# Optimization experiments

Measured on AMD Instinct MI355X. Metric: run time of the kernel, lower is better.

Reference implementation:

```python
import jax, jax.numpy as jnp
import numpy as np

EMB = 384
HID = 256
HEADS = 4
HD = HID // HEADS  # 64
LAYERS = 2
M_DOCS = 32
TOTAL = 4096  # 1 query + 32 docs + 4063 sentences
LN_EPS = 1e-5


def _layernorm(x, scale, bias):
    mu = jnp.mean(x, axis=-1, keepdims=True)
    var = jnp.mean(jnp.square(x - mu), axis=-1, keepdims=True)
    return (x - mu) * jax.lax.rsqrt(var + LN_EPS) * scale + bias


def setup_inputs() -> dict:
    key = jax.random.key(0)
    ks = jax.random.split(key, 12)
    g = 0.05  # small init scale (stand-in for xavier)
    return {
        "node_embeddings": jax.random.normal(ks[0], (TOTAL, EMB), jnp.float32),
        "adj": jax.random.randint(ks[1], (TOTAL, TOTAL), 0, 2, jnp.int32),
        "num_docs": M_DOCS,
        "proj_w": jax.random.normal(ks[2], (HID, EMB), jnp.float32) * g,
        "proj_b": jnp.zeros((HID,), jnp.float32),
        "ln_scale": jnp.ones((LAYERS, HID), jnp.float32),
        "ln_bias": jnp.zeros((LAYERS, HID), jnp.float32),
        "gat_W": jax.random.normal(ks[3], (LAYERS, HEADS, HD, HID), jnp.float32) * g,
        "gat_a": jax.random.normal(ks[4], (LAYERS, HEADS, 2 * HD), jnp.float32) * g,
        "fusion_w": jax.random.normal(ks[5], (HID, 2 * HID + 2), jnp.float32) * g,
        "fusion_b": jnp.zeros((HID,), jnp.float32),
        "out_w": jax.random.normal(ks[6], (HID,), jnp.float32) * g,
        "out_b": jnp.float32(0.5),
    }


def reference(node_embeddings, adj, num_docs, proj_w, proj_b, ln_scale, ln_bias,
              gat_W, gat_a, fusion_w, fusion_b, out_w, out_b):
    T = node_embeddings.shape[0]
    M = num_docs
    N = T - 1 - M  # number of sentences
    # input projection + relu (dropout = identity in eval)
    h = jax.nn.relu(node_embeddings @ proj_w.T + proj_b)  # (T, HID)
    # query-guided sentence re-weighting
    q = h[0:1]                     # (1, HID)
    s = h[1 + M:]                  # (N, HID)
    qn = q / (jnp.linalg.norm(q, axis=1, keepdims=True) + 1e-8)
    sn = s / (jnp.linalg.norm(s, axis=1, keepdims=True) + 1e-8)
    cos = (qn @ sn.T).reshape(-1, 1)          # (N,1)
    s = s + 0.8 * q * cos
    h = jnp.concatenate([h[:1 + M], s], axis=0)
    mask = (adj == 0)[None]                   # (1,T,T)
    for i in range(LAYERS):
        res = h
        x = _layernorm(h, ln_scale[i], ln_bias[i])
        Wh = jnp.einsum('nd,hkd->hnk', x, gat_W[i])                # (H,T,HD)
        # concat-attention a.[Wh_i ; Wh_j] == a_src.Wh_i + a_dst.Wh_j
        src = jnp.einsum('hnk,hk->hn', Wh, gat_a[i, :, :HD])       # (H,T)
        dst = jnp.einsum('hnk,hk->hn', Wh, gat_a[i, :, HD:])       # (H,T)
        e = jax.nn.leaky_relu(src[:, :, None] + dst[:, None, :], 0.2)  # (H,T,T)
        e = jnp.where(mask, -jnp.inf, e)
        attn = jax.nn.softmax(e, axis=-1)                          # softmax over j
        hn = jnp.einsum('hij,hjk->hik', attn, Wh)                  # (H,T,HD)
        hcat = jnp.transpose(hn, (1, 0, 2)).reshape(T, HEADS * HD)
        h = 0.5 * jax.nn.relu(hcat) + 0.5 * res
    qh = h[0:1]
    sh = h[1 + M:]
    scores = (qh @ sh.T) / (HID ** 0.5)       # (1,N)
    aw = jax.nn.softmax(scores, axis=-1)
    awT = aw.T                                # (N,1)
    qw = qh * (awT + 0.5)                     # (N,HID)
    qnf = qh / (jnp.linalg.norm(qh, axis=1, keepdims=True) + 1e-8)
    snf = sh / (jnp.linalg.norm(sh, axis=1, keepdims=True) + 1e-8)
    cosf = (qnf @ snf.T).reshape(-1, 1)       # (N,1)
    feat = jnp.concatenate([sh, qw, cosf, awT], axis=1)  # (N, 2*HID+2)
    g = jax.nn.relu(feat @ fusion_w.T + fusion_b)
    out = g @ out_w + out_b                   # (N,)
    return out + 0.5 * cosf[:, 0]
```

## Files before the change

kernel.cpp:

```cpp
#include <hip/hip_runtime.h>
#include <hip/hip_bf16.h>
#include <stdint.h>

#define TOTAL 4096
#define EMB 384
#define MD 32
#define NDOCS (TOTAL - 1 - MD)
#define LN_EPS 1e-5f

typedef __hip_bfloat16 bf16;
typedef unsigned short ushort_t;
typedef __attribute__((ext_vector_type(8))) short short8;
typedef __attribute__((ext_vector_type(4))) float f32x4;
typedef __attribute__((ext_vector_type(2))) float f32x2;

__device__ __forceinline__ float ldf(const void* p, int i, int isbf) {
    return isbf ? __bfloat162float(((const bf16*)p)[i]) : ((const float*)p)[i];
}

__device__ __forceinline__ unsigned f2bf(float x) {
    return (__float_as_uint(x) + 0x8000u) >> 16;
}

__device__ __forceinline__ unsigned fenc(float f) {
    unsigned u = __float_as_uint(f);
    return (u >> 31) ? ~u : (u | 0x80000000u);
}
__device__ __forceinline__ float fdec(unsigned k) {
    return __uint_as_float((k & 0x80000000u) ? (k & 0x7FFFFFFFu) : ~k);
}

#define NTRANS ((EMB * 256 + 2 * 65536 + 514 * 256) / 256)
__global__ void k_adjmask(const int* adj, unsigned long long* maskb,
                          const uint16_t* embp, int* flag, unsigned* dmaxu,
                          const void* proj_w, const void* gat_W, const void* fusion_w,
                          float* projT, float* gatT, float* fwT) {
    __shared__ int red[4];
    int i = blockIdx.x, t = threadIdx.x;
    int w = t >> 6, l = t & 63;
    for (int c = w; c < 64; c += 4) {
        int a = adj[(size_t)i * TOTAL + c * 64 + l];
        unsigned long long m = __ballot(a != 0);
        if (l == 0) maskb[i * 64 + c] = m;
    }
    if (i == 0) {
        for (int idx = t; idx < 2048; idx += 256) dmaxu[idx] = 0x007FFFFFu;
    }
    if (i < NTRANS) {
        int cnt = 0;
        for (int k = t; k < 4096; k += 256) {
            uint16_t wd = embp[2 * k];
            int e = (wd >> 7) & 0xFF;
            if (e >= 100 && e <= 140) cnt++;
        }
        for (int o = 32; o > 0; o >>= 1) cnt += __shfl_down(cnt, o);
        if ((t & 63) == 0) red[t >> 6] = cnt;
        __syncthreads();
        int isbf = (red[0] + red[1] + red[2] + red[3] > 2048) ? 1 : 0;
        if (i == 0 && t == 0) flag[0] = isbf;
        int idx = i * 256 + t;
        if (idx < EMB * 256) {
            int d = idx >> 8, c = idx & 255;
            projT[idx] = ldf(proj_w, c * EMB + d, isbf);
        } else if (idx < EMB * 256 + 2 * 65536) {
            int r = idx - EMB * 256;
            int ll = r >> 16, rem = r & 65535;
            int d = rem >> 8, c = rem & 255;
            gatT[r] = ldf(gat_W, ll * 65536 + c * 256 + d, isbf);
        } else {
            int r = idx - (EMB * 256 + 2 * 65536);
            int j = r >> 8, c = r & 255;
            fwT[r] = ldf(fusion_w, c * 514 + j, isbf);
        }
    }
}

#define PR 8
__global__ void k_proj(const void* emb, const void* proj_b, const float* projT, float* h,
                       const int* flagp) {
    __shared__ float xs[PR][EMB];
    int isbf = flagp[0];
    int i0 = blockIdx.x * PR, t = threadIdx.x;
    for (int idx = t; idx < PR * EMB; idx += 256) {
        int r = idx / EMB, d = idx % EMB;
        xs[r][d] = ldf(emb, (i0 + r) * EMB + d, isbf);
    }
    __syncthreads();
    float acc[PR];
    float bias = ldf(proj_b, t, isbf);
#pragma unroll
    for (int r = 0; r < PR; r++) acc[r] = bias;
    for (int d0 = 0; d0 < EMB; d0 += 4) {
        float w0 = projT[d0 * 256 + t];
        float w1 = projT[(d0 + 1) * 256 + t];
        float w2 = projT[(d0 + 2) * 256 + t];
        float w3 = projT[(d0 + 3) * 256 + t];
#pragma unroll
        for (int r = 0; r < PR; r++) {
            float4 x = *(const float4*)&xs[r][d0];
            acc[r] = fmaf(x.x, w0, acc[r]);
            acc[r] = fmaf(x.y, w1, acc[r]);
            acc[r] = fmaf(x.z, w2, acc[r]);
            acc[r] = fmaf(x.w, w3, acc[r]);
        }
    }
#pragma unroll
    for (int r = 0; r < PR; r++) h[(size_t)(i0 + r) * 256 + t] = fmaxf(acc[r], 0.f);
}

__global__ __launch_bounds__(256) void k_cosupdate(float* h) {
    int t = threadIdx.x, W = t >> 6, lane = t & 63;
    float4* h4 = (float4*)h;
    float4 q4 = h4[lane];
    float a = q4.x * q4.x + q4.y * q4.y + q4.z * q4.z + q4.w * q4.w;
    for (int o = 32; o > 0; o >>= 1) a += __shfl_xor(a, o);
    float qn = sqrtf(a) + 1e-8f;
    int gw = blockIdx.x * 4 + W;
    for (int n = gw; n < NDOCS; n += 1024) {
        size_t ro = (size_t)(1 + MD + n) * 64;
        float4 s4 = h4[ro + lane];
        float b = s4.x * s4.x + s4.y * s4.y + s4.z * s4.z + s4.w * s4.w;
        float c = q4.x * s4.x + q4.y * s4.y + q4.z * s4.z + q4.w * s4.w;
        for (int o = 32; o > 0; o >>= 1) { b += __shfl_xor(b, o); c += __shfl_xor(c, o); }
        float k = 0.8f * (c / (qn * (sqrtf(b) + 1e-8f)));
        s4.x += k * q4.x; s4.y += k * q4.y; s4.z += k * q4.z; s4.w += k * q4.w;
        h4[ro + lane] = s4;
    }
}

#define LR 4
__global__ void k_ln_wh(float* h, const float* gatT, const void* ln_scale,
                        const void* ln_bias, const void* gat_a,
                        ushort_t* whswz, float* srcb, unsigned* d12g, unsigned* dmaxu,
                        const float* hnp, const float* lpart, int layer, int doepi,
                        const int* flagp) {
    __shared__ float xs[LR][256];
    __shared__ float red[2][LR][4];
    int isbf = flagp[0];
    int i0 = blockIdx.x * LR, t = threadIdx.x;
    int w = t >> 6, l = t & 63;
    float scale = ldf(ln_scale, layer * 256 + t, isbf);
    float bias = ldf(ln_bias, layer * 256 + t, isbf);
    float hv[LR];
    if (doepi) {
#pragma unroll
        for (int r = 0; r < LR; r++) {
            int i = i0 + r;
            float lsum = lpart[(size_t)w * 4096 + i] + lpart[(size_t)(4 + w) * 4096 + i] +
                         lpart[(size_t)(8 + w) * 4096 + i] + lpart[(size_t)(12 + w) * 4096 + i];
            float s = hnp[(size_t)i * 256 + t] + hnp[(size_t)TOTAL * 256 + i * 256 + t] +
                      hnp[(size_t)2 * TOTAL * 256 + i * 256 + t] +
                      hnp[(size_t)3 * TOTAL * 256 + i * 256 + t];
            float hn = 0.5f * fmaxf(s / lsum, 0.f) + 0.5f * h[(size_t)i * 256 + t];
            hv[r] = hn;
            h[(size_t)i * 256 + t] = hn;
        }
    } else {
#pragma unroll
        for (int r = 0; r < LR; r++) hv[r] = h[(size_t)(i0 + r) * 256 + t];
    }
#pragma unroll
    for (int r = 0; r < LR; r++) {
        float a = hv[r], b = hv[r] * hv[r];
        for (int o = 32; o > 0; o >>= 1) { a += __shfl_down(a, o); b += __shfl_down(b, o); }
        if (l == 0) { red[0][r][w] = a; red[1][r][w] = b; }
    }
    __syncthreads();
#pragma unroll
    for (int r = 0; r < LR; r++) {
        float mu = (red[0][r][0] + red[0][r][1] + red[0][r][2] + red[0][r][3]) * (1.f / 256.f);
        float var = (red[1][r][0] + red[1][r][1] + red[1][r][2] + red[1][r][3]) * (1.f / 256.f) - mu * mu;
        float x = (hv[r] - mu) * rsqrtf(var + LN_EPS) * scale + bias;
        xs[r][t] = x;
    }
    __syncthreads();
    const float* gT = gatT + layer * 65536;
    float acc[LR] = {0.f, 0.f, 0.f, 0.f};
    for (int d0 = 0; d0 < 256; d0 += 4) {
        float w0 = gT[d0 * 256 + t];
        float w1 = gT[(d0 + 1) * 256 + t];
        float w2 = gT[(d0 + 2) * 256 + t];
        float w3 = gT[(d0 + 3) * 256 + t];
#pragma unroll
        for (int r = 0; r < LR; r++) {
            float4 x = *(const float4*)&xs[r][d0];
            acc[r] = fmaf(x.x, w0, acc[r]);
            acc[r] = fmaf(x.y, w1, acc[r]);
            acc[r] = fmaf(x.z, w2, acc[r]);
            acc[r] = fmaf(x.w, w3, acc[r]);
        }
    }
    float av1 = ldf(gat_a, layer * 512 + w * 128 + l, isbf);
    float av2 = ldf(gat_a, layer * 512 + w * 128 + 64 + l, isbf);
    const float LOG2E = 1.44269504f;
    float mmax = -__builtin_inff();
#pragma unroll
    for (int r = 0; r < LR; r++) {
        int i = i0 + r;
        int off = (i >> 6) * 16384 + (t >> 6) * 4096 + ((i >> 3) & 7) * 512 +
                  ((t >> 4) & 3) * 128 + (t & 15) * 8 + (i & 7);
        whswz[off] = (ushort_t)f2bf(acc[r]);
        float sv = acc[r] * av1, dv = acc[r] * av2;
        for (int o = 32; o > 0; o >>= 1) { sv += __shfl_down(sv, o); dv += __shfl_down(dv, o); }
        if (l == 0) {
            srcb[w * 4096 + i] = sv;
            float D1 = exp2f(dv * LOG2E), D2 = exp2f(0.2f * dv * LOG2E);
            d12g[w * 4096 + i] = (f2bf(D2) << 16) | f2bf(D1);
            mmax = fmaxf(mmax, dv);
        }
    }
    if (l == 0) atomicMax(&dmaxu[(blockIdx.x & 63) * 16 + w], fenc(mmax));
}

#define TI 32
#define JS 4
__global__ __launch_bounds__(512) void k_pv(const ushort_t* whswz, const float* srcb,
                                            const unsigned* dmaxu, const unsigned* d12g,
                                            const unsigned long long* maskb,
                                            float* hnp, float* lpart) {
    __shared__ __align__(16) char smem[32768];
    __shared__ __align__(16) float lsh[4][2][4][4];
    __shared__ unsigned mlut[4];
    __shared__ float dmx[4];
    unsigned* d12s = (unsigned*)smem;
    unsigned long long* mbs = (unsigned long long*)(smem + 16384);
    float* srcs = (float*)(smem + 16384 + 4352);
    f32x4* accsh = (f32x4*)smem;
    int t = threadIdx.x;
    int W = t >> 6, lane = t & 63;
    int h = W & 3, kq = W >> 2;
    int quad = lane >> 4, c16 = lane & 15;
    int i0 = blockIdx.x * TI;
    int jbase = blockIdx.y * 1024;
    if (t < 4) mlut[t] = (t & 1 ? 0x0000FFFFu : 0u) | (t & 2 ? 0xFFFF0000u : 0u);
    if (t < 256) {
        int hh = t >> 6, sl = t & 63;
        float v = fdec(dmaxu[sl * 16 + hh]);
        for (int o = 32; o > 0; o >>= 1) v = fmaxf(v, __shfl_xor(v, o));
        if (sl == 0) dmx[hh] = v;
    }
    for (int idx = t; idx < TI * 16; idx += 512) {
        int r = idx >> 4, wd = idx & 15;
        mbs[r * 17 + wd] = maskb[(size_t)(i0 + r) * 64 + (jbase >> 6) + wd];
    }
    for (int idx = t; idx < 1024; idx += 512) {
        int hh = idx >> 8, j4 = idx & 255;
        ((uint4*)d12s)[idx] = ((const uint4*)(d12g + hh * 4096 + jbase))[j4];
    }
    if (t < 128) {
        int h2 = t >> 5, r = t & 31;
        srcs[h2 * 32 + r] = srcb[h2 * 4096 + i0 + r];
    }
    __syncthreads();
    const float LOG2E = 1.44269504f;
    float dm = dmx[h];
    float E1[2], E2[2];
#pragma unroll
    for (int rt = 0; rt < 2; rt++) {
        float src = srcs[h * 32 + rt * 16 + c16];
        float sd = src + dm;
        float rce = -fmaxf(sd, 0.2f * sd);
        E1[rt] = exp2f((src + rce) * LOG2E);
        E2[rt] = exp2f((0.2f * src + rce) * LOG2E);
    }
    f32x4 acc[2][4];
    f32x4 accl[2] = {(f32x4){0.f, 0.f, 0.f, 0.f}, (f32x4){0.f, 0.f, 0.f, 0.f}};
#pragma unroll
    for (int rt = 0; rt < 2; rt++)
#pragma unroll
        for (int ct = 0; ct < 4; ct++) acc[rt][ct] = (f32x4){0.f, 0.f, 0.f, 0.f};
    uint4 onesu;
    unsigned os = (c16 == 0) ? 0x3F803F80u : 0u;
    onesu.x = os; onesu.y = os; onesu.z = os; onesu.w = os;
    short8 bfones = __builtin_bit_cast(short8, onesu);
    const uint4* g4 = (const uint4*)whswz;
    size_t b0 = (size_t)(jbase >> 6) * 2048 + h * 512 + (kq * 4 + quad) * 64 + c16;
    uint4 bn[4];
#pragma unroll
    for (int ct = 0; ct < 4; ct++) bn[ct] = g4[b0 + ct * 16];
    for (int step = 0; step < 16; step++) {
        uint4 bc[4];
#pragma unroll
        for (int ct = 0; ct < 4; ct++) bc[ct] = bn[ct];
        if (step < 15) {
            size_t bs = b0 + (size_t)(step + 1) * 2048;
#pragma unroll
            for (int ct = 0; ct < 4; ct++) bn[ct] = g4[bs + ct * 16];
        }
        int jl0 = step * 64 + kq * 32 + quad * 8;
        unsigned mby[2];
#pragma unroll
        for (int rt = 0; rt < 2; rt++)
            mby[rt] = (unsigned)(mbs[(rt * 16 + c16) * 17 + step] >> (kq * 32 + quad * 8)) & 0xFFu;
        const uint4* dj = (const uint4*)&d12s[h * 1024 + jl0];
        uint4 da = dj[0], db = dj[1];
        unsigned dw[8] = {da.x, da.y, da.z, da.w, db.x, db.y, db.z, db.w};
        f32x2 D1[4], D2[4];
#pragma unroll
        for (int q = 0; q < 4; q++) {
            unsigned a = dw[2 * q], b = dw[2 * q + 1];
            D1[q] = (f32x2){__uint_as_float(a << 16), __uint_as_float(b << 16)};
            D2[q] = (f32x2){__uint_as_float(a & 0xFFFF0000u), __uint_as_float(b & 0xFFFF0000u)};
        }
        uint4 afu[2];
#pragma unroll
        for (int rt = 0; rt < 2; rt++) {
            unsigned pu[4];
#pragma unroll
            for (int q = 0; q < 4; q++) {
                f32x2 v1 = D1[q] * E1[rt];
                f32x2 v2 = D2[q] * E2[rt];
                f32x2 m = __builtin_elementwise_max(v1, v2);
                unsigned v = ((__float_as_uint(m.x) + 0x8000u) >> 16) |
                             ((__float_as_uint(m.y) + 0x8000u) & 0xFFFF0000u);
                pu[q] = v & mlut[(mby[rt] >> (2 * q)) & 3u];
            }
            afu[rt].x = pu[0]; afu[rt].y = pu[1]; afu[rt].z = pu[2]; afu[rt].w = pu[3];
        }
        short8 af0 = __builtin_bit_cast(short8, afu[0]);
        short8 af1 = __builtin_bit_cast(short8, afu[1]);
#pragma unroll
        for (int ct = 0; ct < 4; ct++) {
            short8 bf = __builtin_bit_cast(short8, bc[ct]);
            acc[0][ct] = __builtin_amdgcn_mfma_f32_16x16x32_bf16(af0, bf, acc[0][ct], 0, 0, 0);
            acc[1][ct] = __builtin_amdgcn_mfma_f32_16x16x32_bf16(af1, bf, acc[1][ct], 0, 0, 0);
        }
        accl[0] = __builtin_amdgcn_mfma_f32_16x16x32_bf16(af0, bfones, accl[0], 0, 0, 0);
        accl[1] = __builtin_amdgcn_mfma_f32_16x16x32_bf16(af1, bfones, accl[1], 0, 0, 0);
    }
    __syncthreads();
    if (kq == 1) {
#pragma unroll
        for (int rt = 0; rt < 2; rt++) {
#pragma unroll
            for (int ct = 0; ct < 4; ct++)
                accsh[((h * 2 + rt) * 4 + ct) * 64 + lane] = acc[rt][ct];
            if (c16 == 0) *(f32x4*)&lsh[h][rt][quad][0] = accl[rt];
        }
    }
    __syncthreads();
    if (kq == 0) {
        float* out = hnp + (size_t)blockIdx.y * (TOTAL * 256);
#pragma unroll
        for (int rt = 0; rt < 2; rt++) {
#pragma unroll
            for (int ct = 0; ct < 4; ct++) {
                f32x4 o = acc[rt][ct] + accsh[((h * 2 + rt) * 4 + ct) * 64 + lane];
#pragma unroll
                for (int rr = 0; rr < 4; rr++) {
                    int row = i0 + rt * 16 + quad * 4 + rr;
                    out[(size_t)row * 256 + h * 64 + ct * 16 + c16] = o[rr];
                }
            }
            if (c16 == 0) {
                f32x4 lv = accl[rt] + *(const f32x4*)&lsh[h][rt][quad][0];
#pragma unroll
                for (int rr = 0; rr < 4; rr++)
                    lpart[(size_t)(blockIdx.y * 4 + h) * 4096 + i0 + rt * 16 + quad * 4 + rr] = lv[rr];
            }
        }
    }
}

__global__ __launch_bounds__(256) void k_scores(float* h, const float* hnp, const float* lpart,
                                                float* qrow, float* scoresv, float* cosv) {
    int t = threadIdx.x, W = t >> 6, lane = t & 63;
    int hh = lane >> 4;
    float4* h4 = (float4*)h;
    const float4* p0 = (const float4*)hnp;
    const float4* p1 = p0 + (size_t)TOTAL * 64;
    const float4* p2 = p1 + (size_t)TOTAL * 64;
    const float4* p3 = p2 + (size_t)TOTAL * 64;
    int gw = blockIdx.x * 4 + W;
    float lq = lpart[(size_t)hh * 4096] + lpart[(size_t)(4 + hh) * 4096] +
               lpart[(size_t)(8 + hh) * 4096] + lpart[(size_t)(12 + hh) * 4096];
    float4 a0 = p0[lane], a1 = p1[lane], a2 = p2[lane], a3 = p3[lane];
    float4 hq = h4[lane];
    float invq = 1.f / lq;
    float4 q4;
    q4.x = 0.5f * fmaxf((a0.x + a1.x + a2.x + a3.x) * invq, 0.f) + 0.5f * hq.x;
    q4.y = 0.5f * fmaxf((a0.y + a1.y + a2.y + a3.y) * invq, 0.f) + 0.5f * hq.y;
    q4.z = 0.5f * fmaxf((a0.z + a1.z + a2.z + a3.z) * invq, 0.f) + 0.5f * hq.z;
    q4.w = 0.5f * fmaxf((a0.w + a1.w + a2.w + a3.w) * invq, 0.f) + 0.5f * hq.w;
    if (gw == 0) ((float4*)qrow)[lane] = q4;
    float a = q4.x * q4.x + q4.y * q4.y + q4.z * q4.z + q4.w * q4.w;
    for (int o = 32; o > 0; o >>= 1) a += __shfl_xor(a, o);
    float qn = sqrtf(a) + 1e-8f;
    for (int n = gw; n < NDOCS; n += 1024) {
        int row = 1 + MD + n;
        size_t ro = (size_t)row * 64;
        float ld = lpart[(size_t)hh * 4096 + row] + lpart[(size_t)(4 + hh) * 4096 + row] +
                   lpart[(size_t)(8 + hh) * 4096 + row] + lpart[(size_t)(12 + hh) * 4096 + row];
        float4 b0 = p0[ro + lane], b1 = p1[ro + lane], b2 = p2[ro + lane], b3 = p3[ro + lane];
        float4 ho = h4[ro + lane];
        float invd = 1.f / ld;
        float4 s4;
        s4.x = 0.5f * fmaxf((b0.x + b1.x + b2.x + b3.x) * invd, 0.f) + 0.5f * ho.x;
        s4.y = 0.5f * fmaxf((b0.y + b1.y + b2.y + b3.y) * invd, 0.f) + 0.5f * ho.y;
        s4.z = 0.5f * fmaxf((b0.z + b1.z + b2.z + b3.z) * invd, 0.f) + 0.5f * ho.z;
        s4.w = 0.5f * fmaxf((b0.w + b1.w + b2.w + b3.w) * invd, 0.f) + 0.5f * ho.w;
        h4[ro + lane] = s4;
        float b = s4.x * s4.x + s4.y * s4.y + s4.z * s4.z + s4.w * s4.w;
        float c = q4.x * s4.x + q4.y * s4.y + q4.z * s4.z + q4.w * s4.w;
        for (int o = 32; o > 0; o >>= 1) { b += __shfl_xor(b, o); c += __shfl_xor(c, o); }
        if (lane == 0) {
            scoresv[n] = c * (1.f / 16.f);
            cosv[n] = c / (qn * (sqrtf(b) + 1e-8f));
        }
    }
}

__global__ __launch_bounds__(1024) void k_softmax(const float* scoresv, float* awv) {
    __shared__ float red[16];
    int t = threadIdx.x;
    float m = -__builtin_inff();
    for (int n = t; n < NDOCS; n += 1024) m = fmaxf(m, scoresv[n]);
    for (int o = 32; o > 0; o >>= 1) m = fmaxf(m, __shfl_down(m, o));
    if ((t & 63) == 0) red[t >> 6] = m;
    __syncthreads();
    m = red[0];
#pragma unroll
    for (int i = 1; i < 16; i++) m = fmaxf(m, red[i]);
    __syncthreads();
    float s = 0.f;
    for (int n = t; n < NDOCS; n += 1024) s += __expf(scoresv[n] - m);
    for (int o = 32; o > 0; o >>= 1) s += __shfl_down(s, o);
    if ((t & 63) == 0) red[t >> 6] = s;
    __syncthreads();
    s = 0.f;
#pragma unroll
    for (int i = 0; i < 16; i++) s += red[i];
    float inv = 1.f / s;
    for (int n = t; n < NDOCS; n += 1024) awv[n] = __expf(scoresv[n] - m) * inv;
}

#define TN 8
__global__ __launch_bounds__(256) void k_fusion(const float* h, const float* qrow,
                                                const float* awv, const float* cosv,
                                                const float* fwT, const void* fusion_b,
                                                const void* out_w, const void* out_bp,
                                                void* outv, const int* flagp) {
    __shared__ float feats2[514][TN];
    __shared__ float qhs[256];
    __shared__ float red[TN][4];
    int isbf = flagp[0];
    int t = threadIdx.x;
    int n0 = blockIdx.x * TN;
    qhs[t] = qrow[t];
    __syncthreads();
    for (int idx = t; idx < 514 * TN; idx += 256) {
        int j = idx >> 3, r = idx & 7;
        int n = n0 + r;
        float v = 0.f;
        if (n < NDOCS) {
            if (j < 256) v = h[(size_t)(1 + MD + n) * 256 + j];
            else if (j < 512) v = qhs[j - 256] * (awv[n] + 0.5f);
            else if (j == 512) v = cosv[n];
            else v = awv[n];
        }
        feats2[j][r] = v;
    }
    __syncthreads();
    float acc[TN];
    float bk = ldf(fusion_b, t, isbf);
#pragma unroll
    for (int r = 0; r < TN; r++) acc[r] = bk;
    for (int j0 = 0; j0 < 512; j0 += 8) {
        float wv[8];
#pragma unroll
        for (int u = 0; u < 8; u++) wv[u] = fwT[(j0 + u) * 256 + t];
#pragma unroll
        for (int u = 0; u < 8; u++) {
            float4 fa = *(const float4*)&feats2[j0 + u][0];
            float4 fb = *(const float4*)&feats2[j0 + u][4];
            acc[0] = fmaf(fa.x, wv[u], acc[0]); acc[1] = fmaf(fa.y, wv[u], acc[1]);
            acc[2] = fmaf(fa.z, wv[u], acc[2]); acc[3] = fmaf(fa.w, wv[u], acc[3]);
            acc[4] = fmaf(fb.x, wv[u], acc[4]); acc[5] = fmaf(fb.y, wv[u], acc[5]);
            acc[6] = fmaf(fb.z, wv[u], acc[6]); acc[7] = fmaf(fb.w, wv[u], acc[7]);
        }
    }
#pragma unroll
    for (int j = 512; j < 514; j++) {
        float wv = fwT[j * 256 + t];
#pragma unroll
        for (int r = 0; r < TN; r++) acc[r] = fmaf(feats2[j][r], wv, acc[r]);
    }
    float ow = ldf(out_w, t, isbf);
    float outb = ldf(out_bp, 0, isbf);
#pragma unroll
    for (int r = 0; r < TN; r++) {
        float o = fmaxf(acc[r], 0.f) * ow;
        for (int off = 32; off > 0; off >>= 1) o += __shfl_down(o, off);
        if ((t & 63) == 0) red[r][t >> 6] = o;
    }
    __syncthreads();
    if (t < TN) {
        int n = n0 + t;
        if (n < NDOCS) {
            float o = red[t][0] + red[t][1] + red[t][2] + red[t][3] + outb + 0.5f * cosv[n];
            if (isbf) ((bf16*)outv)[n] = __float2bfloat16(o);
            else      ((float*)outv)[n] = o;
        }
    }
}

extern "C" void kernel_launch(void* const* d_in, const int* in_sizes, int n_in,
                              void* d_out, int out_size, void* d_ws, size_t ws_size,
                              hipStream_t stream) {
    const void* emb      = d_in[0];
    const int*  adj      = (const int*)d_in[1];
    const void* proj_w   = d_in[3];
    const void* proj_b   = d_in[4];
    const void* ln_scale = d_in[5];
    const void* ln_bias  = d_in[6];
    const void* gat_W    = d_in[7];
    const void* gat_a    = d_in[8];
    const void* fusion_w = d_in[9];
    const void* fusion_b = d_in[10];
    const void* out_w    = d_in[11];
    const void* out_b    = d_in[12];

    unsigned long long* maskb = (unsigned long long*)d_ws;
    int* flag = (int*)((char*)d_ws + (size_t)4096 * 64 * 8);
    float* f = (float*)((char*)d_ws + (size_t)4096 * 64 * 8 + 256);
    float* h       = f; f += 4096 * 256;
    float* srcb    = f; f += 4 * 4096;
    unsigned* d12g = (unsigned*)f; f += 4 * 4096;
    unsigned* dmaxu = (unsigned*)f; f += 2048;
    float* projT   = f; f += EMB * 256;
    float* gatT    = f; f += 2 * 65536;
    float* fwT     = f; f += 514 * 256;
    float* scoresv = f; f += 4096;
    float* cosv    = f; f += 4096;
    float* awv     = f; f += 4096;
    float* qrow    = f; f += 256;
    float* lpart   = f; f += 4 * 4 * 4096;
    ushort_t* whswz = (ushort_t*)f; f += 4096 * 256 / 2;
    float* hnp     = f; f += (size_t)JS * 4096 * 256;

    k_adjmask<<<dim3(4096), dim3(256), 0, stream>>>(adj, maskb, (const uint16_t*)emb, flag,
                                                    dmaxu, proj_w, gat_W, fusion_w,
                                                    projT, gatT, fwT);
    k_proj<<<dim3(TOTAL / PR), dim3(256), 0, stream>>>(emb, proj_b, projT, h, flag);
    k_cosupdate<<<dim3(256), dim3(256), 0, stream>>>(h);
    for (int layer = 0; layer < 2; layer++) {
        k_ln_wh<<<dim3(TOTAL / LR), dim3(256), 0, stream>>>(h, gatT, ln_scale, ln_bias, gat_a,
                                                            whswz, srcb, d12g, dmaxu + layer * 1024,
                                                            hnp, lpart, layer, layer, flag);
        k_pv<<<dim3(TOTAL / TI, JS), dim3(512), 0, stream>>>(whswz, srcb, dmaxu + layer * 1024,
                                                             d12g, maskb, hnp, lpart);
    }
    k_scores<<<dim3(256), dim3(256), 0, stream>>>(h, hnp, lpart, qrow, scoresv, cosv);
    k_softmax<<<dim3(1), dim3(1024), 0, stream>>>(scoresv, awv);
    k_fusion<<<dim3((NDOCS + TN - 1) / TN), dim3(256), 0, stream>>>(h, qrow, awv, cosv,
                                                                    fwT, fusion_b, out_w,
                                                                    out_b, (void*)d_out, flag);
}
```

Before: 304.0 us.

## Fuse all stages into one persistent megakernel with grid-wide barriers

Replaces the chain of separate launches (adjacency mask, projection, cosine update, per-layer LN/Wh and attention PV, scores, softmax, fusion) with one persistent kernel of 256 blocks of 512 threads. The stages are separated by software grid barriers built on atomics. The attention j-split is cut from 4 to 2 partial buffers, which shrinks the hnp and lpart workspace. This removes launch overhead and inter-kernel gaps, but reduces parallelism per stage and relies on all blocks being co-resident. The spin barrier gives up after a bounded number of spins, so it can silently proceed before every block arrives.

```diff
diff --git a/kernel.cpp b/kernel.cpp
--- a/kernel.cpp
+++ b/kernel.cpp
@@ -7,6 +7,8 @@
 #define MD 32
 #define NDOCS (TOTAL - 1 - MD)
 #define LN_EPS 1e-5f
+#define NBLK 256
+#define NTHR 512
 
 typedef __hip_bfloat16 bf16;
 typedef unsigned short ushort_t;
@@ -17,11 +19,9 @@
 __device__ __forceinline__ float ldf(const void* p, int i, int isbf) {
     return isbf ? __bfloat162float(((const bf16*)p)[i]) : ((const float*)p)[i];
 }
-
 __device__ __forceinline__ unsigned f2bf(float x) {
     return (__float_as_uint(x) + 0x8000u) >> 16;
 }
-
 __device__ __forceinline__ unsigned fenc(float f) {
     unsigned u = __float_as_uint(f);
     return (u >> 31) ? ~u : (u | 0x80000000u);
@@ -30,476 +30,518 @@
     return __uint_as_float((k & 0x80000000u) ? (k & 0x7FFFFFFFu) : ~k);
 }
 
-#define NTRANS ((EMB * 256 + 2 * 65536 + 514 * 256) / 256)
-__global__ void k_adjmask(const int* adj, unsigned long long* maskb,
-                          const uint16_t* embp, int* flag, unsigned* dmaxu,
-                          const void* proj_w, const void* gat_W, const void* fusion_w,
-                          float* projT, float* gatT, float* fwT) {
-    __shared__ int red[4];
-    int i = blockIdx.x, t = threadIdx.x;
-    int w = t >> 6, l = t & 63;
-    for (int c = w; c < 64; c += 4) {
-        int a = adj[(size_t)i * TOTAL + c * 64 + l];
-        unsigned long long m = __ballot(a != 0);
-        if (l == 0) maskb[i * 64 + c] = m;
-    }
-    if (i == 0) {
-        for (int idx = t; idx < 2048; idx += 256) dmaxu[idx] = 0x007FFFFFu;
-    }
-    if (i < NTRANS) {
+__device__ __forceinline__ void gbar(unsigned* barr, int k) {
+    __syncthreads();
+    if (threadIdx.x == 0) {
+        unsigned* c = barr + k * 32;
+        __hip_atomic_fetch_add(c, 1u, __ATOMIC_ACQ_REL, __HIP_MEMORY_SCOPE_AGENT);
+        int spins = 0;
+        while (__hip_atomic_load(c, __ATOMIC_RELAXED, __HIP_MEMORY_SCOPE_AGENT) < NBLK &&
+               spins < 50000) {
+            __builtin_amdgcn_s_sleep(8);
+            spins++;
+        }
+        __threadfence();
+    }
+    __syncthreads();
+}
+
+#define NTOT (EMB * 256 + 2 * 65536 + 514 * 256)
+
+__global__ __launch_bounds__(NTHR, 2) void k_mega(
+    const int* adj, const void* emb, const void* proj_w, const void* gat_W,
+    const void* fusion_w, const void* proj_b, const void* ln_scale, const void* ln_bias,
+    const void* gat_a, const void* fusion_b, const void* out_w, const void* out_bp,
+    void* outv, unsigned* barr,
+    unsigned long long* maskb, unsigned* dmaxu,
+    float* projT, float* gatT, float* fwT,
+    float* h, float* srcb, unsigned* d12g, ushort_t* whswz,
+    float* hnp, float* lpart, float* scoresv, float* cosv, float* awv, float* qrow) {
+    __shared__ __align__(16) char arena[33344];
+    int t = threadIdx.x, b = blockIdx.x;
+    int wv_ = t >> 6, lane = t & 63;
+    const float LOG2E = 1.44269504f;
+
+    int isbf;
+    {
+        int* red = (int*)arena;
         int cnt = 0;
-        for (int k = t; k < 4096; k += 256) {
-            uint16_t wd = embp[2 * k];
+        for (int k = t; k < 4096; k += NTHR) {
+            uint16_t wd = ((const uint16_t*)emb)[2 * k];
             int e = (wd >> 7) & 0xFF;
-            if (e >= 100 && e <= 140) cnt++;
+            cnt += (e >= 100 && e <= 140);
         }
         for (int o = 32; o > 0; o >>= 1) cnt += __shfl_down(cnt, o);
-        if ((t & 63) == 0) red[t >> 6] = cnt;
-        __syncthreads();
-        int isbf = (red[0] + red[1] + red[2] + red[3] > 2048) ? 1 : 0;
-        if (i == 0 && t == 0) flag[0] = isbf;
-        int idx = i * 256 + t;
-        if (idx < EMB * 256) {
-            int d = idx >> 8, c = idx & 255;
-            projT[idx] = ldf(proj_w, c * EMB + d, isbf);
-        } else if (idx < EMB * 256 + 2 * 65536) {
-            int r = idx - EMB * 256;
-            int ll = r >> 16, rem = r & 65535;
-            int d = rem >> 8, c = rem & 255;
-            gatT[r] = ldf(gat_W, ll * 65536 + c * 256 + d, isbf);
-        } else {
-            int r = idx - (EMB * 256 + 2 * 65536);
-            int j = r >> 8, c = r & 255;
-            fwT[r] = ldf(fusion_w, c * 514 + j, isbf);
-        }
-    }
-}
-
-#define PR 8
-__global__ void k_proj(const void* emb, const void* proj_b, const float* projT, float* h,
-                       const int* flagp) {
-    __shared__ float xs[PR][EMB];
-    int isbf = flagp[0];
-    int i0 = blockIdx.x * PR, t = threadIdx.x;
-    for (int idx = t; idx < PR * EMB; idx += 256) {
-        int r = idx / EMB, d = idx % EMB;
-        xs[r][d] = ldf(emb, (i0 + r) * EMB + d, isbf);
-    }
-    __syncthreads();
-    float acc[PR];
-    float bias = ldf(proj_b, t, isbf);
-#pragma unroll
-    for (int r = 0; r < PR; r++) acc[r] = bias;
-    for (int d0 = 0; d0 < EMB; d0 += 4) {
-        float w0 = projT[d0 * 256 + t];
-        float w1 = projT[(d0 + 1) * 256 + t];
-        float w2 = projT[(d0 + 2) * 256 + t];
-        float w3 = projT[(d0 + 3) * 256 + t];
-#pragma unroll
-        for (int r = 0; r < PR; r++) {
-            float4 x = *(const float4*)&xs[r][d0];
-            acc[r] = fmaf(x.x, w0, acc[r]);
-            acc[r] = fmaf(x.y, w1, acc[r]);
-            acc[r] = fmaf(x.z, w2, acc[r]);
-            acc[r] = fmaf(x.w, w3, acc[r]);
-        }
-    }
-#pragma unroll
-    for (int r = 0; r < PR; r++) h[(size_t)(i0 + r) * 256 + t] = fmaxf(acc[r], 0.f);
-}
-
-__global__ __launch_bounds__(256) void k_cosupdate(float* h) {
-    int t = threadIdx.x, W = t >> 6, lane = t & 63;
-    float4* h4 = (float4*)h;
-    float4 q4 = h4[lane];
-    float a = q4.x * q4.x + q4.y * q4.y + q4.z * q4.z + q4.w * q4.w;
-    for (int o = 32; o > 0; o >>= 1) a += __shfl_xor(a, o);
-    float qn = sqrtf(a) + 1e-8f;
-    int gw = blockIdx.x * 4 + W;
-    for (int n = gw; n < NDOCS; n += 1024) {
-        size_t ro = (size_t)(1 + MD + n) * 64;
-        float4 s4 = h4[ro + lane];
-        float b = s4.x * s4.x + s4.y * s4.y + s4.z * s4.z + s4.w * s4.w;
-        float c = q4.x * s4.x + q4.y * s4.y + q4.z * s4.z + q4.w * s4.w;
-        for (int o = 32; o > 0; o >>= 1) { b += __shfl_xor(b, o); c += __shfl_xor(c, o); }
-        float k = 0.8f * (c / (qn * (sqrtf(b) + 1e-8f)));
-        s4.x += k * q4.x; s4.y += k * q4.y; s4.z += k * q4.z; s4.w += k * q4.w;
-        h4[ro + lane] = s4;
-    }
-}
-
-#define LR 4
-__global__ void k_ln_wh(float* h, const float* gatT, const void* ln_scale,
-                        const void* ln_bias, const void* gat_a,
-                        ushort_t* whswz, float* srcb, unsigned* d12g, unsigned* dmaxu,
-                        const float* hnp, const float* lpart, int layer, int doepi,
-                        const int* flagp) {
-    __shared__ float xs[LR][256];
-    __shared__ float red[2][LR][4];
-    int isbf = flagp[0];
-    int i0 = blockIdx.x * LR, t = threadIdx.x;
-    int w = t >> 6, l = t & 63;
-    float scale = ldf(ln_scale, layer * 256 + t, isbf);
-    float bias = ldf(ln_bias, layer * 256 + t, isbf);
-    float hv[LR];
-    if (doepi) {
-#pragma unroll
-        for (int r = 0; r < LR; r++) {
-            int i = i0 + r;
-            float lsum = lpart[(size_t)w * 4096 + i] + lpart[(size_t)(4 + w) * 4096 + i] +
-                         lpart[(size_t)(8 + w) * 4096 + i] + lpart[(size_t)(12 + w) * 4096 + i];
-            float s = hnp[(size_t)i * 256 + t] + hnp[(size_t)TOTAL * 256 + i * 256 + t] +
-                      hnp[(size_t)2 * TOTAL * 256 + i * 256 + t] +
-                      hnp[(size_t)3 * TOTAL * 256 + i * 256 + t];
-            float hn = 0.5f * fmaxf(s / lsum, 0.f) + 0.5f * h[(size_t)i * 256 + t];
-            hv[r] = hn;
-            h[(size_t)i * 256 + t] = hn;
-        }
-    } else {
-#pragma unroll
-        for (int r = 0; r < LR; r++) hv[r] = h[(size_t)(i0 + r) * 256 + t];
-    }
-#pragma unroll
-    for (int r = 0; r < LR; r++) {
-        float a = hv[r], b = hv[r] * hv[r];
-        for (int o = 32; o > 0; o >>= 1) { a += __shfl_down(a, o); b += __shfl_down(b, o); }
-        if (l == 0) { red[0][r][w] = a; red[1][r][w] = b; }
-    }
-    __syncthreads();
-#pragma unroll
-    for (int r = 0; r < LR; r++) {
-        float mu = (red[0][r][0] + red[0][r][1] + red[0][r][2] + red[0][r][3]) * (1.f / 256.f);
-        float var = (red[1][r][0] + red[1][r][1] + red[1][r][2] + red[1][r][3]) * (1.f / 256.f) - mu * mu;
-        float x = (hv[r] - mu) * rsqrtf(var + LN_EPS) * scale + bias;
-        xs[r][t] = x;
-    }
-    __syncthreads();
-    const float* gT = gatT + layer * 65536;
-    float acc[LR] = {0.f, 0.f, 0.f, 0.f};
-    for (int d0 = 0; d0 < 256; d0 += 4) {
-        float w0 = gT[d0 * 256 + t];
-        float w1 = gT[(d0 + 1) * 256 + t];
-        float w2 = gT[(d0 + 2) * 256 + t];
-        float w3 = gT[(d0 + 3) * 256 + t];
-#pragma unroll
-        for (int r = 0; r < LR; r++) {
-            float4 x = *(const float4*)&xs[r][d0];
-            acc[r] = fmaf(x.x, w0, acc[r]);
-            acc[r] = fmaf(x.y, w1, acc[r]);
-            acc[r] = fmaf(x.z, w2, acc[r]);
-            acc[r] = fmaf(x.w, w3, acc[r]);
-        }
-    }
-    float av1 = ldf(gat_a, layer * 512 + w * 128 + l, isbf);
-    float av2 = ldf(gat_a, layer * 512 + w * 128 + 64 + l, isbf);
-    const float LOG2E = 1.44269504f;
-    float mmax = -__builtin_inff();
-#pragma unroll
-    for (int r = 0; r < LR; r++) {
-        int i = i0 + r;
-        int off = (i >> 6) * 16384 + (t >> 6) * 4096 + ((i >> 3) & 7) * 512 +
-                  ((t >> 4) & 3) * 128 + (t & 15) * 8 + (i & 7);
-        whswz[off] = (ushort_t)f2bf(acc[r]);
-        float sv = acc[r] * av1, dv = acc[r] * av2;
-        for (int o = 32; o > 0; o >>= 1) { sv += __shfl_down(sv, o); dv += __shfl_down(dv, o); }
-        if (l == 0) {
-            srcb[w * 4096 + i] = sv;
-            float D1 = exp2f(dv * LOG2E), D2 = exp2f(0.2f * dv * LOG2E);
-            d12g[w * 4096 + i] = (f2bf(D2) << 16) | f2bf(D1);
-            mmax = fmaxf(mmax, dv);
-        }
-    }
-    if (l == 0) atomicMax(&dmaxu[(blockIdx.x & 63) * 16 + w], fenc(mmax));
-}
-
-#define TI 32
-#define JS 4
-__global__ __launch_bounds__(512) void k_pv(const ushort_t* whswz, const float* srcb,
-                                            const unsigned* dmaxu, const unsigned* d12g,
-                                            const unsigned long long* maskb,
-                                            float* hnp, float* lpart) {
-    __shared__ __align__(16) char smem[32768];
-    __shared__ __align__(16) float lsh[4][2][4][4];
-    __shared__ unsigned mlut[4];
-    __shared__ float dmx[4];
-    unsigned* d12s = (unsigned*)smem;
-    unsigned long long* mbs = (unsigned long long*)(smem + 16384);
-    float* srcs = (float*)(smem + 16384 + 4352);
-    f32x4* accsh = (f32x4*)smem;
-    int t = threadIdx.x;
-    int W = t >> 6, lane = t & 63;
-    int h = W & 3, kq = W >> 2;
-    int quad = lane >> 4, c16 = lane & 15;
-    int i0 = blockIdx.x * TI;
-    int jbase = blockIdx.y * 1024;
-    if (t < 4) mlut[t] = (t & 1 ? 0x0000FFFFu : 0u) | (t & 2 ? 0xFFFF0000u : 0u);
-    if (t < 256) {
-        int hh = t >> 6, sl = t & 63;
-        float v = fdec(dmaxu[sl * 16 + hh]);
-        for (int o = 32; o > 0; o >>= 1) v = fmaxf(v, __shfl_xor(v, o));
-        if (sl == 0) dmx[hh] = v;
-    }
-    for (int idx = t; idx < TI * 16; idx += 512) {
-        int r = idx >> 4, wd = idx & 15;
-        mbs[r * 17 + wd] = maskb[(size_t)(i0 + r) * 64 + (jbase >> 6) + wd];
-    }
-    for (int idx = t; idx < 1024; idx += 512) {
-        int hh = idx >> 8, j4 = idx & 255;
-        ((uint4*)d12s)[idx] = ((const uint4*)(d12g + hh * 4096 + jbase))[j4];
-    }
-    if (t < 128) {
-        int h2 = t >> 5, r = t & 31;
-        srcs[h2 * 32 + r] = srcb[h2 * 4096 + i0 + r];
-    }
-    __syncthreads();
-    const float LOG2E = 1.44269504f;
-    float dm = dmx[h];
-    float E1[2], E2[2];
-#pragma unroll
-    for (int rt = 0; rt < 2; rt++) {
-        float src = srcs[h * 32 + rt * 16 + c16];
-        float sd = src + dm;
-        float rce = -fmaxf(sd, 0.2f * sd);
-        E1[rt] = exp2f((src + rce) * LOG2E);
-        E2[rt] = exp2f((0.2f * src + rce) * LOG2E);
-    }
-    f32x4 acc[2][4];
-    f32x4 accl[2] = {(f32x4){0.f, 0.f, 0.f, 0.f}, (f32x4){0.f, 0.f, 0.f, 0.f}};
-#pragma unroll
-    for (int rt = 0; rt < 2; rt++)
-#pragma unroll
-        for (int ct = 0; ct < 4; ct++) acc[rt][ct] = (f32x4){0.f, 0.f, 0.f, 0.f};
-    uint4 onesu;
-    unsigned os = (c16 == 0) ? 0x3F803F80u : 0u;
-    onesu.x = os; onesu.y = os; onesu.z = os; onesu.w = os;
-    short8 bfones = __builtin_bit_cast(short8, onesu);
-    const uint4* g4 = (const uint4*)whswz;
-    size_t b0 = (size_t)(jbase >> 6) * 2048 + h * 512 + (kq * 4 + quad) * 64 + c16;
-    uint4 bn[4];
-#pragma unroll
-    for (int ct = 0; ct < 4; ct++) bn[ct] = g4[b0 + ct * 16];
-    for (int step = 0; step < 16; step++) {
-        uint4 bc[4];
-#pragma unroll
-        for (int ct = 0; ct < 4; ct++) bc[ct] = bn[ct];
-        if (step < 15) {
-            size_t bs = b0 + (size_t)(step + 1) * 2048;
-#pragma unroll
-            for (int ct = 0; ct < 4; ct++) bn[ct] = g4[bs + ct * 16];
-        }
-        int jl0 = step * 64 + kq * 32 + quad * 8;
-        unsigned mby[2];
-#pragma unroll
-        for (int rt = 0; rt < 2; rt++)
-            mby[rt] = (unsigned)(mbs[(rt * 16 + c16) * 17 + step] >> (kq * 32 + quad * 8)) & 0xFFu;
-        const uint4* dj = (const uint4*)&d12s[h * 1024 + jl0];
-        uint4 da = dj[0], db = dj[1];
-        unsigned dw[8] = {da.x, da.y, da.z, da.w, db.x, db.y, db.z, db.w};
-        f32x2 D1[4], D2[4];
-#pragma unroll
-        for (int q = 0; q < 4; q++) {
-            unsigned a = dw[2 * q], b = dw[2 * q + 1];
-            D1[q] = (f32x2){__uint_as_float(a << 16), __uint_as_float(b << 16)};
-            D2[q] = (f32x2){__uint_as_float(a & 0xFFFF0000u), __uint_as_float(b & 0xFFFF0000u)};
-        }
-        uint4 afu[2];
-#pragma unroll
-        for (int rt = 0; rt < 2; rt++) {
-            unsigned pu[4];
-#pragma unroll
-            for (int q = 0; q < 4; q++) {
-                f32x2 v1 = D1[q] * E1[rt];
-                f32x2 v2 = D2[q] * E2[rt];
-                f32x2 m = __builtin_elementwise_max(v1, v2);
-                unsigned v = ((__float_as_uint(m.x) + 0x8000u) >> 16) |
-                             ((__float_as_uint(m.y) + 0x8000u) & 0xFFFF0000u);
-                pu[q] = v & mlut[(mby[rt] >> (2 * q)) & 3u];
-            }
-            afu[rt].x = pu[0]; afu[rt].y = pu[1]; afu[rt].z = pu[2]; afu[rt].w = pu[3];
-        }
-        short8 af0 = __builtin_bit_cast(short8, afu[0]);
-        short8 af1 = __builtin_bit_cast(short8, afu[1]);
-#pragma unroll
-        for (int ct = 0; ct < 4; ct++) {
-            short8 bf = __builtin_bit_cast(short8, bc[ct]);
-            acc[0][ct] = __builtin_amdgcn_mfma_f32_16x16x32_bf16(af0, bf, acc[0][ct], 0, 0, 0);
-            acc[1][ct] = __builtin_amdgcn_mfma_f32_16x16x32_bf16(af1, bf, acc[1][ct], 0, 0, 0);
-        }
-        accl[0] = __builtin_amdgcn_mfma_f32_16x16x32_bf16(af0, bfones, accl[0], 0, 0, 0);
-        accl[1] = __builtin_amdgcn_mfma_f32_16x16x32_bf16(af1, bfones, accl[1], 0, 0, 0);
-    }
-    __syncthreads();
-    if (kq == 1) {
-#pragma unroll
-        for (int rt = 0; rt < 2; rt++) {
-#pragma unroll
-            for (int ct = 0; ct < 4; ct++)
-                accsh[((h * 2 + rt) * 4 + ct) * 64 + lane] = acc[rt][ct];
-            if (c16 == 0) *(f32x4*)&lsh[h][rt][quad][0] = accl[rt];
-        }
-    }
-    __syncthreads();
-    if (kq == 0) {
-        float* out = hnp + (size_t)blockIdx.y * (TOTAL * 256);
-#pragma unroll
-        for (int rt = 0; rt < 2; rt++) {
-#pragma unroll
-            for (int ct = 0; ct < 4; ct++) {
-                f32x4 o = acc[rt][ct] + accsh[((h * 2 + rt) * 4 + ct) * 64 + lane];
-#pragma unroll
-                for (int rr = 0; rr < 4; rr++) {
-                    int row = i0 + rt * 16 + quad * 4 + rr;
-                    out[(size_t)row * 256 + h * 64 + ct * 16 + c16] = o[rr];
-                }
-            }
-            if (c16 == 0) {
-                f32x4 lv = accl[rt] + *(const f32x4*)&lsh[h][rt][quad][0];
-#pragma unroll
-                for (int rr = 0; rr < 4; rr++)
-                    lpart[(size_t)(blockIdx.y * 4 + h) * 4096 + i0 + rt * 16 + quad * 4 + rr] = lv[rr];
-            }
-        }
-    }
-}
-
-__global__ __launch_bounds__(256) void k_scores(float* h, const float* hnp, const float* lpart,
-                                                float* qrow, float* scoresv, float* cosv) {
-    int t = threadIdx.x, W = t >> 6, lane = t & 63;
-    int hh = lane >> 4;
-    float4* h4 = (float4*)h;
-    const float4* p0 = (const float4*)hnp;
-    const float4* p1 = p0 + (size_t)TOTAL * 64;
-    const float4* p2 = p1 + (size_t)TOTAL * 64;
-    const float4* p3 = p2 + (size_t)TOTAL * 64;
-    int gw = blockIdx.x * 4 + W;
-    float lq = lpart[(size_t)hh * 4096] + lpart[(size_t)(4 + hh) * 4096] +
-               lpart[(size_t)(8 + hh) * 4096] + lpart[(size_t)(12 + hh) * 4096];
-    float4 a0 = p0[lane], a1 = p1[lane], a2 = p2[lane], a3 = p3[lane];
-    float4 hq = h4[lane];
-    float invq = 1.f / lq;
-    float4 q4;
-    q4.x = 0.5f * fmaxf((a0.x + a1.x + a2.x + a3.x) * invq, 0.f) + 0.5f * hq.x;
-    q4.y = 0.5f * fmaxf((a0.y + a1.y + a2.y + a3.y) * invq, 0.f) + 0.5f * hq.y;
-    q4.z = 0.5f * fmaxf((a0.z + a1.z + a2.z + a3.z) * invq, 0.f) + 0.5f * hq.z;
-    q4.w = 0.5f * fmaxf((a0.w + a1.w + a2.w + a3.w) * invq, 0.f) + 0.5f * hq.w;
-    if (gw == 0) ((float4*)qrow)[lane] = q4;
-    float a = q4.x * q4.x + q4.y * q4.y + q4.z * q4.z + q4.w * q4.w;
-    for (int o = 32; o > 0; o >>= 1) a += __shfl_xor(a, o);
-    float qn = sqrtf(a) + 1e-8f;
-    for (int n = gw; n < NDOCS; n += 1024) {
-        int row = 1 + MD + n;
-        size_t ro = (size_t)row * 64;
-        float ld = lpart[(size_t)hh * 4096 + row] + lpart[(size_t)(4 + hh) * 4096 + row] +
-                   lpart[(size_t)(8 + hh) * 4096 + row] + lpart[(size_t)(12 + hh) * 4096 + row];
-        float4 b0 = p0[ro + lane], b1 = p1[ro + lane], b2 = p2[ro + lane], b3 = p3[ro + lane];
-        float4 ho = h4[ro + lane];
-        float invd = 1.f / ld;
-        float4 s4;
-        s4.x = 0.5f * fmaxf((b0.x + b1.x + b2.x + b3.x) * invd, 0.f) + 0.5f * ho.x;
-        s4.y = 0.5f * fmaxf((b0.y + b1.y + b2.y + b3.y) * invd, 0.f) + 0.5f * ho.y;
-        s4.z = 0.5f * fmaxf((b0.z + b1.z + b2.z + b3.z) * invd, 0.f) + 0.5f * ho.z;
-        s4.w = 0.5f * fmaxf((b0.w + b1.w + b2.w + b3.w) * invd, 0.f) + 0.5f * ho.w;
-        h4[ro + lane] = s4;
-        float b = s4.x * s4.x + s4.y * s4.y + s4.z * s4.z + s4.w * s4.w;
-        float c = q4.x * s4.x + q4.y * s4.y + q4.z * s4.z + q4.w * s4.w;
-        for (int o = 32; o > 0; o >>= 1) { b += __shfl_xor(b, o); c += __shfl_xor(c, o); }
-        if (lane == 0) {
-            scoresv[n] = c * (1.f / 16.f);
-            cosv[n] = c / (qn * (sqrtf(b) + 1e-8f));
-        }
-    }
-}
-
-__global__ __launch_bounds__(1024) void k_softmax(const float* scoresv, float* awv) {
-    __shared__ float red[16];
-    int t = threadIdx.x;
-    float m = -__builtin_inff();
-    for (int n = t; n < NDOCS; n += 1024) m = fmaxf(m, scoresv[n]);
-    for (int o = 32; o > 0; o >>= 1) m = fmaxf(m, __shfl_down(m, o));
-    if ((t & 63) == 0) red[t >> 6] = m;
-    __syncthreads();
-    m = red[0];
-#pragma unroll
-    for (int i = 1; i < 16; i++) m = fmaxf(m, red[i]);
-    __syncthreads();
-    float s = 0.f;
-    for (int n = t; n < NDOCS; n += 1024) s += __expf(scoresv[n] - m);
-    for (int o = 32; o > 0; o >>= 1) s += __shfl_down(s, o);
-    if ((t & 63) == 0) red[t >> 6] = s;
-    __syncthreads();
-    s = 0.f;
-#pragma unroll
-    for (int i = 0; i < 16; i++) s += red[i];
-    float inv = 1.f / s;
-    for (int n = t; n < NDOCS; n += 1024) awv[n] = __expf(scoresv[n] - m) * inv;
-}
-
-#define TN 8
-__global__ __launch_bounds__(256) void k_fusion(const float* h, const float* qrow,
-                                                const float* awv, const float* cosv,
-                                                const float* fwT, const void* fusion_b,
-                                                const void* out_w, const void* out_bp,
-                                                void* outv, const int* flagp) {
-    __shared__ float feats2[514][TN];
-    __shared__ float qhs[256];
-    __shared__ float red[TN][4];
-    int isbf = flagp[0];
-    int t = threadIdx.x;
-    int n0 = blockIdx.x * TN;
-    qhs[t] = qrow[t];
-    __syncthreads();
-    for (int idx = t; idx < 514 * TN; idx += 256) {
-        int j = idx >> 3, r = idx & 7;
-        int n = n0 + r;
-        float v = 0.f;
-        if (n < NDOCS) {
-            if (j < 256) v = h[(size_t)(1 + MD + n) * 256 + j];
-            else if (j < 512) v = qhs[j - 256] * (awv[n] + 0.5f);
-            else if (j == 512) v = cosv[n];
-            else v = awv[n];
-        }
-        feats2[j][r] = v;
-    }
-    __syncthreads();
-    float acc[TN];
-    float bk = ldf(fusion_b, t, isbf);
-#pragma unroll
-    for (int r = 0; r < TN; r++) acc[r] = bk;
-    for (int j0 = 0; j0 < 512; j0 += 8) {
-        float wv[8];
-#pragma unroll
-        for (int u = 0; u < 8; u++) wv[u] = fwT[(j0 + u) * 256 + t];
-#pragma unroll
-        for (int u = 0; u < 8; u++) {
-            float4 fa = *(const float4*)&feats2[j0 + u][0];
-            float4 fb = *(const float4*)&feats2[j0 + u][4];
-            acc[0] = fmaf(fa.x, wv[u], acc[0]); acc[1] = fmaf(fa.y, wv[u], acc[1]);
-            acc[2] = fmaf(fa.z, wv[u], acc[2]); acc[3] = fmaf(fa.w, wv[u], acc[3]);
-            acc[4] = fmaf(fb.x, wv[u], acc[4]); acc[5] = fmaf(fb.y, wv[u], acc[5]);
-            acc[6] = fmaf(fb.z, wv[u], acc[6]); acc[7] = fmaf(fb.w, wv[u], acc[7]);
-        }
-    }
-#pragma unroll
-    for (int j = 512; j < 514; j++) {
-        float wv = fwT[j * 256 + t];
-#pragma unroll
-        for (int r = 0; r < TN; r++) acc[r] = fmaf(feats2[j][r], wv, acc[r]);
-    }
-    float ow = ldf(out_w, t, isbf);
-    float outb = ldf(out_bp, 0, isbf);
-#pragma unroll
-    for (int r = 0; r < TN; r++) {
-        float o = fmaxf(acc[r], 0.f) * ow;
-        for (int off = 32; off > 0; off >>= 1) o += __shfl_down(o, off);
-        if ((t & 63) == 0) red[r][t >> 6] = o;
-    }
-    __syncthreads();
-    if (t < TN) {
-        int n = n0 + t;
-        if (n < NDOCS) {
-            float o = red[t][0] + red[t][1] + red[t][2] + red[t][3] + outb + 0.5f * cosv[n];
-            if (isbf) ((bf16*)outv)[n] = __float2bfloat16(o);
-            else      ((float*)outv)[n] = o;
+        if (lane == 0) red[wv_] = cnt;
+        __syncthreads();
+        int tot = 0;
+#pragma unroll
+        for (int i = 0; i < 8; i++) tot += red[i];
+        isbf = tot > 2048;
+        __syncthreads();
+    }
+
+    {
+        int row0 = b * 16 + wv_ * 2;
+#pragma unroll
+        for (int rr = 0; rr < 2; rr++) {
+            int row = row0 + rr;
+            for (int c0 = 0; c0 < 64; c0 += 8) {
+                int a[8];
+#pragma unroll
+                for (int u = 0; u < 8; u++) a[u] = adj[(size_t)row * TOTAL + (c0 + u) * 64 + lane];
+#pragma unroll
+                for (int u = 0; u < 8; u++) {
+                    unsigned long long m = __ballot(a[u] != 0);
+                    if (lane == 0) maskb[row * 64 + c0 + u] = m;
+                }
+            }
+        }
+        if (b == 0) for (int idx = t; idx < 2048; idx += NTHR) dmaxu[idx] = 0x007FFFFFu;
+        for (int idx = b * NTHR + t; idx < NTOT; idx += NBLK * NTHR) {
+            if (idx < EMB * 256) {
+                int d = idx >> 8, c = idx & 255;
+                projT[idx] = ldf(proj_w, c * EMB + d, isbf);
+            } else if (idx < EMB * 256 + 2 * 65536) {
+                int r = idx - EMB * 256;
+                int ll = r >> 16, rem = r & 65535;
+                int d = rem >> 8, c = rem & 255;
+                gatT[r] = ldf(gat_W, ll * 65536 + c * 256 + d, isbf);
+            } else {
+                int r = idx - (EMB * 256 + 2 * 65536);
+                int j = r >> 8, c = r & 255;
+                fwT[r] = ldf(fusion_w, c * 514 + j, isbf);
+            }
+        }
+    }
+    gbar(barr, 0);
+
+    {
+        float* xs = (float*)arena;
+        int col = t & 255, g = t >> 8;
+        int i0 = b * 16;
+        for (int idx = t; idx < 16 * EMB; idx += NTHR) {
+            int r = idx / EMB, d = idx - r * EMB;
+            xs[r * EMB + d] = ldf(emb, (i0 + r) * EMB + d, isbf);
+        }
+        __syncthreads();
+        float acc[8];
+        float bias = ldf(proj_b, col, isbf);
+#pragma unroll
+        for (int r = 0; r < 8; r++) acc[r] = bias;
+        for (int d0 = 0; d0 < EMB; d0 += 4) {
+            float w0 = projT[d0 * 256 + col];
+            float w1 = projT[(d0 + 1) * 256 + col];
+            float w2 = projT[(d0 + 2) * 256 + col];
+            float w3 = projT[(d0 + 3) * 256 + col];
+#pragma unroll
+            for (int r = 0; r < 8; r++) {
+                float4 x = *(const float4*)&xs[(g * 8 + r) * EMB + d0];
+                acc[r] = fmaf(x.x, w0, acc[r]); acc[r] = fmaf(x.y, w1, acc[r]);
+                acc[r] = fmaf(x.z, w2, acc[r]); acc[r] = fmaf(x.w, w3, acc[r]);
+            }
+        }
+#pragma unroll
+        for (int r = 0; r < 8; r++)
+            h[(size_t)(i0 + g * 8 + r) * 256 + col] = fmaxf(acc[r], 0.f);
+    }
+    gbar(barr, 1);
+
+    {
+        float4* h4 = (float4*)h;
+        float4 q4 = h4[lane];
+        float a = q4.x * q4.x + q4.y * q4.y + q4.z * q4.z + q4.w * q4.w;
+        for (int o = 32; o > 0; o >>= 1) a += __shfl_xor(a, o);
+        float qn = sqrtf(a) + 1e-8f;
+#pragma unroll
+        for (int v = 0; v < 2; v++) {
+            int n = v * 2048 + b * 8 + wv_;
+            if (n < NDOCS) {
+                size_t ro = (size_t)(1 + MD + n) * 64;
+                float4 s4 = h4[ro + lane];
+                float bb = s4.x * s4.x + s4.y * s4.y + s4.z * s4.z + s4.w * s4.w;
+                float cc = q4.x * s4.x + q4.y * s4.y + q4.z * s4.z + q4.w * s4.w;
+                for (int o = 32; o > 0; o >>= 1) { bb += __shfl_xor(bb, o); cc += __shfl_xor(cc, o); }
+                float k = 0.8f * (cc / (qn * (sqrtf(bb) + 1e-8f)));
+                s4.x += k * q4.x; s4.y += k * q4.y; s4.z += k * q4.z; s4.w += k * q4.w;
+                h4[ro + lane] = s4;
+            }
+        }
+    }
+    gbar(barr, 2);
+
+    for (int layer = 0; layer < 2; layer++) {
+        {
+            float* xs = (float*)arena;
+            float* redA = (float*)(arena + 16384);
+            float* redB = (float*)(arena + 16640);
+            unsigned* dml = dmaxu + layer * 1024;
+            int col = t & 255, g = t >> 8, head = col >> 6, w4 = wv_ & 3;
+            int i0 = b * 16;
+            float scale = ldf(ln_scale, layer * 256 + col, isbf);
+            float bias = ldf(ln_bias, layer * 256 + col, isbf);
+            float hv[8];
+            if (layer == 1) {
+#pragma unroll
+                for (int r = 0; r < 8; r++) {
+                    int i = i0 + g * 8 + r;
+                    float lsum = lpart[(size_t)head * 4096 + i] +
+                                 lpart[(size_t)(4 + head) * 4096 + i];
+                    float s = hnp[(size_t)i * 256 + col] +
+                              hnp[(size_t)TOTAL * 256 + i * 256 + col];
+                    float hn = 0.5f * fmaxf(s / lsum, 0.f) + 0.5f * h[(size_t)i * 256 + col];
+                    hv[r] = hn;
+                    h[(size_t)i * 256 + col] = hn;
+                }
+            } else {
+#pragma unroll
+                for (int r = 0; r < 8; r++) hv[r] = h[(size_t)(i0 + g * 8 + r) * 256 + col];
+            }
+#pragma unroll
+            for (int r = 0; r < 8; r++) {
+                float a = hv[r], bsq = hv[r] * hv[r];
+                for (int o = 32; o > 0; o >>= 1) { a += __shfl_down(a, o); bsq += __shfl_down(bsq, o); }
+                if (lane == 0) { redA[(g * 8 + r) * 4 + w4] = a; redB[(g * 8 + r) * 4 + w4] = bsq; }
+            }
+            __syncthreads();
+#pragma unroll
+            for (int r = 0; r < 8; r++) {
+                int rr = g * 8 + r;
+                float mu = (redA[rr * 4] + redA[rr * 4 + 1] + redA[rr * 4 + 2] + redA[rr * 4 + 3]) * (1.f / 256.f);
+                float var = (redB[rr * 4] + redB[rr * 4 + 1] + redB[rr * 4 + 2] + redB[rr * 4 + 3]) * (1.f / 256.f) - mu * mu;
+                xs[rr * 256 + col] = (hv[r] - mu) * rsqrtf(var + LN_EPS) * scale + bias;
+            }
+            __syncthreads();
+            const float* gT = gatT + layer * 65536;
+            float acc[8] = {0.f, 0.f, 0.f, 0.f, 0.f, 0.f, 0.f, 0.f};
+            for (int d0 = 0; d0 < 256; d0 += 4) {
+                float w0 = gT[d0 * 256 + col];
+                float w1 = gT[(d0 + 1) * 256 + col];
+                float w2 = gT[(d0 + 2) * 256 + col];
+                float w3 = gT[(d0 + 3) * 256 + col];
+#pragma unroll
+                for (int r = 0; r < 8; r++) {
+                    float4 x = *(const float4*)&xs[(g * 8 + r) * 256 + d0];
+                    acc[r] = fmaf(x.x, w0, acc[r]); acc[r] = fmaf(x.y, w1, acc[r]);
+                    acc[r] = fmaf(x.z, w2, acc[r]); acc[r] = fmaf(x.w, w3, acc[r]);
+                }
+            }
+            float av1 = ldf(gat_a, layer * 512 + head * 128 + (col & 63), isbf);
+            float av2 = ldf(gat_a, layer * 512 + head * 128 + 64 + (col & 63), isbf);
+            float mmax = -__builtin_inff();
+#pragma unroll
+            for (int r = 0; r < 8; r++) {
+                int i = i0 + g * 8 + r;
+                int off = (i >> 6) * 16384 + head * 4096 + ((i >> 3) & 7) * 512 +
+                          ((col >> 4) & 3) * 128 + (col & 15) * 8 + (i & 7);
+                whswz[off] = (ushort_t)f2bf(acc[r]);
+                float sv = acc[r] * av1, dv = acc[r] * av2;
+                for (int o = 32; o > 0; o >>= 1) { sv += __shfl_down(sv, o); dv += __shfl_down(dv, o); }
+                if (lane == 0) {
+                    srcb[head * 4096 + i] = sv;
+                    float D1 = exp2f(dv * LOG2E), D2 = exp2f(0.2f * dv * LOG2E);
+                    d12g[head * 4096 + i] = (f2bf(D2) << 16) | f2bf(D1);
+                    mmax = fmaxf(mmax, dv);
+                }
+            }
+            if (lane == 0) atomicMax(&dml[(b & 63) * 16 + head], fenc(mmax));
+        }
+        gbar(barr, 3 + layer * 2);
+
+        {
+            unsigned* d12s = (unsigned*)arena;
+            unsigned long long* mbs = (unsigned long long*)(arena + 16384);
+            float* srcs = (float*)(arena + 24832);
+            f32x4* accsh = (f32x4*)arena;
+            float* lsh = (float*)(arena + 32768);
+            unsigned* mlut = (unsigned*)(arena + 33280);
+            float* dmx = (float*)(arena + 33296);
+            const unsigned* dml = dmaxu + layer * 1024;
+            int it = b & 127, js = b >> 7;
+            int hh = wv_ & 3, kq = wv_ >> 2;
+            int quad = lane >> 4, c16 = lane & 15;
+            int i0 = it * 32;
+            int jb0 = js * 2048;
+            if (t < 4) mlut[t] = (t & 1 ? 0x0000FFFFu : 0u) | (t & 2 ? 0xFFFF0000u : 0u);
+            if (t < 256) {
+                int h2 = t >> 6, sl = t & 63;
+                float v = fdec(dml[sl * 16 + h2]);
+                for (int o = 32; o > 0; o >>= 1) v = fmaxf(v, __shfl_xor(v, o));
+                if (sl == 0) dmx[h2] = v;
+            }
+            for (int idx = t; idx < 32 * 32; idx += NTHR) {
+                int r = idx >> 5, wd = idx & 31;
+                mbs[r * 33 + wd] = maskb[(size_t)(i0 + r) * 64 + (jb0 >> 6) + wd];
+            }
+            if (t < 128) {
+                int h2 = t >> 5, r = t & 31;
+                srcs[h2 * 32 + r] = srcb[h2 * 4096 + i0 + r];
+            }
+            __syncthreads();
+            float dm = dmx[hh];
+            float E1[2], E2[2];
+#pragma unroll
+            for (int rt = 0; rt < 2; rt++) {
+                float src = srcs[hh * 32 + rt * 16 + c16];
+                float sd = src + dm;
+                float rce = -fmaxf(sd, 0.2f * sd);
+                E1[rt] = exp2f((src + rce) * LOG2E);
+                E2[rt] = exp2f((0.2f * src + rce) * LOG2E);
+            }
+            f32x4 acc[2][4];
+            f32x4 accl[2] = {(f32x4){0.f, 0.f, 0.f, 0.f}, (f32x4){0.f, 0.f, 0.f, 0.f}};
+#pragma unroll
+            for (int rt = 0; rt < 2; rt++)
+#pragma unroll
+                for (int ct = 0; ct < 4; ct++) acc[rt][ct] = (f32x4){0.f, 0.f, 0.f, 0.f};
+            uint4 onesu;
+            unsigned os = (c16 == 0) ? 0x3F803F80u : 0u;
+            onesu.x = os; onesu.y = os; onesu.z = os; onesu.w = os;
+            short8 bfones = __builtin_bit_cast(short8, onesu);
+            const uint4* g4 = (const uint4*)whswz;
+            for (int half = 0; half < 2; half++) {
+                if (half) __syncthreads();
+                for (int idx = t; idx < 1024; idx += NTHR) {
+                    int h2 = idx >> 8, j4 = idx & 255;
+                    ((uint4*)d12s)[idx] = ((const uint4*)(d12g + h2 * 4096 + jb0 + half * 1024))[j4];
+                }
+                __syncthreads();
+                size_t b0 = (size_t)((jb0 + half * 1024) >> 6) * 2048 + hh * 512 +
+                            (kq * 4 + quad) * 64 + c16;
+                uint4 bn[4];
+#pragma unroll
+                for (int ct = 0; ct < 4; ct++) bn[ct] = g4[b0 + ct * 16];
+                for (int step = 0; step < 16; step++) {
+                    uint4 bc[4];
+#pragma unroll
+                    for (int ct = 0; ct < 4; ct++) bc[ct] = bn[ct];
+                    if (step < 15) {
+                        size_t bs = b0 + (size_t)(step + 1) * 2048;
+#pragma unroll
+                        for (int ct = 0; ct < 4; ct++) bn[ct] = g4[bs + ct * 16];
+                    }
+                    int jl0 = step * 64 + kq * 32 + quad * 8;
+                    unsigned mby[2];
+#pragma unroll
+                    for (int rt = 0; rt < 2; rt++)
+                        mby[rt] = (unsigned)(mbs[(rt * 16 + c16) * 33 + half * 16 + step] >>
+                                             (kq * 32 + quad * 8)) & 0xFFu;
+                    const uint4* dj = (const uint4*)&d12s[hh * 1024 + jl0];
+                    uint4 da = dj[0], db = dj[1];
+                    unsigned dw[8] = {da.x, da.y, da.z, da.w, db.x, db.y, db.z, db.w};
+                    f32x2 D1[4], D2[4];
+#pragma unroll
+                    for (int q = 0; q < 4; q++) {
+                        unsigned a = dw[2 * q], bb = dw[2 * q + 1];
+                        D1[q] = (f32x2){__uint_as_float(a << 16), __uint_as_float(bb << 16)};
+                        D2[q] = (f32x2){__uint_as_float(a & 0xFFFF0000u), __uint_as_float(bb & 0xFFFF0000u)};
+                    }
+                    uint4 afu[2];
+#pragma unroll
+                    for (int rt = 0; rt < 2; rt++) {
+                        unsigned pu[4];
+#pragma unroll
+                        for (int q = 0; q < 4; q++) {
+                            f32x2 v1 = D1[q] * E1[rt];
+                            f32x2 v2 = D2[q] * E2[rt];
+                            f32x2 m = __builtin_elementwise_max(v1, v2);
+                            unsigned v = ((__float_as_uint(m.x) + 0x8000u) >> 16) |
+                                         ((__float_as_uint(m.y) + 0x8000u) & 0xFFFF0000u);
+                            pu[q] = v & mlut[(mby[rt] >> (2 * q)) & 3u];
+                        }
+                        afu[rt].x = pu[0]; afu[rt].y = pu[1]; afu[rt].z = pu[2]; afu[rt].w = pu[3];
+                    }
+                    short8 af0 = __builtin_bit_cast(short8, afu[0]);
+                    short8 af1 = __builtin_bit_cast(short8, afu[1]);
+#pragma unroll
+                    for (int ct = 0; ct < 4; ct++) {
+                        short8 bf = __builtin_bit_cast(short8, bc[ct]);
+                        acc[0][ct] = __builtin_amdgcn_mfma_f32_16x16x32_bf16(af0, bf, acc[0][ct], 0, 0, 0);
+                        acc[1][ct] = __builtin_amdgcn_mfma_f32_16x16x32_bf16(af1, bf, acc[1][ct], 0, 0, 0);
+                    }
+                    accl[0] = __builtin_amdgcn_mfma_f32_16x16x32_bf16(af0, bfones, accl[0], 0, 0, 0);
+                    accl[1] = __builtin_amdgcn_mfma_f32_16x16x32_bf16(af1, bfones, accl[1], 0, 0, 0);
+                }
+            }
+            __syncthreads();
+            if (kq == 1) {
+#pragma unroll
+                for (int rt = 0; rt < 2; rt++) {
+#pragma unroll
+                    for (int ct = 0; ct < 4; ct++)
+                        accsh[((hh * 2 + rt) * 4 + ct) * 64 + lane] = acc[rt][ct];
+                    if (c16 == 0) *(f32x4*)&lsh[((hh * 2 + rt) * 4 + quad) * 4] = accl[rt];
+                }
+            }
+            __syncthreads();
+            if (kq == 0) {
+                float* out = hnp + (size_t)js * (TOTAL * 256);
+#pragma unroll
+                for (int rt = 0; rt < 2; rt++) {
+#pragma unroll
+                    for (int ct = 0; ct < 4; ct++) {
+                        f32x4 o = acc[rt][ct] + accsh[((hh * 2 + rt) * 4 + ct) * 64 + lane];
+#pragma unroll
+                        for (int rr = 0; rr < 4; rr++) {
+                            int row = i0 + rt * 16 + quad * 4 + rr;
+                            out[(size_t)row * 256 + hh * 64 + ct * 16 + c16] = o[rr];
+                        }
+                    }
+                    if (c16 == 0) {
+                        f32x4 lv = accl[rt] + *(const f32x4*)&lsh[((hh * 2 + rt) * 4 + quad) * 4];
+#pragma unroll
+                        for (int rr = 0; rr < 4; rr++)
+                            lpart[(size_t)(js * 4 + hh) * 4096 + i0 + rt * 16 + quad * 4 + rr] = lv[rr];
+                    }
+                }
+            }
+        }
+        gbar(barr, 4 + layer * 2);
+    }
+
+    {
+        int hh = lane >> 4;
+        float4* h4 = (float4*)h;
+        const float4* p0 = (const float4*)hnp;
+        const float4* p1 = p0 + (size_t)TOTAL * 64;
+        int gw = b * 8 + wv_;
+        float lq = lpart[(size_t)hh * 4096] + lpart[(size_t)(4 + hh) * 4096];
+        float4 a0 = p0[lane], a1 = p1[lane];
+        float4 hq = h4[lane];
+        float invq = 1.f / lq;
+        float4 q4;
+        q4.x = 0.5f * fmaxf((a0.x + a1.x) * invq, 0.f) + 0.5f * hq.x;
+        q4.y = 0.5f * fmaxf((a0.y + a1.y) * invq, 0.f) + 0.5f * hq.y;
+        q4.z = 0.5f * fmaxf((a0.z + a1.z) * invq, 0.f) + 0.5f * hq.z;
+        q4.w = 0.5f * fmaxf((a0.w + a1.w) * invq, 0.f) + 0.5f * hq.w;
+        if (gw == 0) ((float4*)qrow)[lane] = q4;
+        float a = q4.x * q4.x + q4.y * q4.y + q4.z * q4.z + q4.w * q4.w;
+        for (int o = 32; o > 0; o >>= 1) a += __shfl_xor(a, o);
+        float qn = sqrtf(a) + 1e-8f;
+#pragma unroll
+        for (int v = 0; v < 2; v++) {
+            int n = v * 2048 + gw;
+            if (n < NDOCS) {
+                int row = 1 + MD + n;
+                size_t ro = (size_t)row * 64;
+                float ld = lpart[(size_t)hh * 4096 + row] + lpart[(size_t)(4 + hh) * 4096 + row];
+                float4 b0 = p0[ro + lane], b1 = p1[ro + lane];
+                float4 ho = h4[ro + lane];
+                float invd = 1.f / ld;
+                float4 s4;
+                s4.x = 0.5f * fmaxf((b0.x + b1.x) * invd, 0.f) + 0.5f * ho.x;
+                s4.y = 0.5f * fmaxf((b0.y + b1.y) * invd, 0.f) + 0.5f * ho.y;
+                s4.z = 0.5f * fmaxf((b0.z + b1.z) * invd, 0.f) + 0.5f * ho.z;
+                s4.w = 0.5f * fmaxf((b0.w + b1.w) * invd, 0.f) + 0.5f * ho.w;
+                h4[ro + lane] = s4;
+                float bb = s4.x * s4.x + s4.y * s4.y + s4.z * s4.z + s4.w * s4.w;
+                float cc = q4.x * s4.x + q4.y * s4.y + q4.z * s4.z + q4.w * s4.w;
+                for (int o = 32; o > 0; o >>= 1) { bb += __shfl_xor(bb, o); cc += __shfl_xor(cc, o); }
+                if (lane == 0) {
+                    scoresv[n] = cc * (1.f / 16.f);
+                    cosv[n] = cc / (qn * (sqrtf(bb) + 1e-8f));
+                }
+            }
+        }
+    }
+    gbar(barr, 7);
+
+    if (b == 0) {
+        float* red = (float*)arena;
+        float m = -__builtin_inff();
+        for (int n = t; n < NDOCS; n += NTHR) m = fmaxf(m, scoresv[n]);
+        for (int o = 32; o > 0; o >>= 1) m = fmaxf(m, __shfl_down(m, o));
+        if (lane == 0) red[wv_] = m;
+        __syncthreads();
+        m = red[0];
+#pragma unroll
+        for (int i = 1; i < 8; i++) m = fmaxf(m, red[i]);
+        __syncthreads();
+        float s = 0.f;
+        for (int n = t; n < NDOCS; n += NTHR) s += __expf(scoresv[n] - m);
+        for (int o = 32; o > 0; o >>= 1) s += __shfl_down(s, o);
+        if (lane == 0) red[wv_] = s;
+        __syncthreads();
+        s = 0.f;
+#pragma unroll
+        for (int i = 0; i < 8; i++) s += red[i];
+        float inv = 1.f / s;
+        for (int n = t; n < NDOCS; n += NTHR) awv[n] = __expf(scoresv[n] - m) * inv;
+    }
+    gbar(barr, 8);
+
+    for (int v = 0; v < 2; v++) {
+        float* feats2 = (float*)arena;
+        float* qhs = (float*)(arena + 16448);
+        float* redr = (float*)(arena + 17472);
+        float* redc = (float*)(arena + 17600);
+        int col = t & 255, g = t >> 8;
+        int n0 = (v * 256 + b) * 8;
+        __syncthreads();
+        if (t < 256) qhs[t] = qrow[t];
+        __syncthreads();
+        for (int idx = t; idx < 514 * 8; idx += NTHR) {
+            int j = idx >> 3, r = idx & 7;
+            int n = n0 + r;
+            float vv = 0.f;
+            if (n < NDOCS) {
+                if (j < 256) vv = h[(size_t)(1 + MD + n) * 256 + j];
+                else if (j < 512) vv = qhs[j - 256] * (awv[n] + 0.5f);
+                else if (j == 512) vv = cosv[n];
+                else vv = awv[n];
+            }
+            feats2[j * 8 + r] = vv;
+        }
+        __syncthreads();
+        float acc[8];
+        float bk = (g == 0) ? ldf(fusion_b, col, isbf) : 0.f;
+#pragma unroll
+        for (int r = 0; r < 8; r++) acc[r] = bk;
+        int jlo = g * 256;
+        for (int j0 = jlo; j0 < jlo + 256; j0 += 8) {
+            float wv[8];
+#pragma unroll
+            for (int u = 0; u < 8; u++) wv[u] = fwT[(j0 + u) * 256 + col];
+#pragma unroll
+            for (int u = 0; u < 8; u++) {
+                float4 fa = *(const float4*)&feats2[(j0 + u) * 8];
+                float4 fb = *(const float4*)&feats2[(j0 + u) * 8 + 4];
+                acc[0] = fmaf(fa.x, wv[u], acc[0]); acc[1] = fmaf(fa.y, wv[u], acc[1]);
+                acc[2] = fmaf(fa.z, wv[u], acc[2]); acc[3] = fmaf(fa.w, wv[u], acc[3]);
+                acc[4] = fmaf(fb.x, wv[u], acc[4]); acc[5] = fmaf(fb.y, wv[u], acc[5]);
+                acc[6] = fmaf(fb.z, wv[u], acc[6]); acc[7] = fmaf(fb.w, wv[u], acc[7]);
+            }
+        }
+        if (g == 1) {
+#pragma unroll
+            for (int j = 512; j < 514; j++) {
+                float wvx = fwT[j * 256 + col];
+#pragma unroll
+                for (int r = 0; r < 8; r++) acc[r] = fmaf(feats2[j * 8 + r], wvx, acc[r]);
+            }
+#pragma unroll
+            for (int r = 0; r < 8; r++) redc[r * 256 + col] = acc[r];
+        }
+        __syncthreads();
+        float ow = ldf(out_w, col, isbf);
+        float outb = ldf(out_bp, 0, isbf);
+        if (g == 0) {
+#pragma unroll
+            for (int r = 0; r < 8; r++) {
+                float o = fmaxf(acc[r] + redc[r * 256 + col], 0.f) * ow;
+                for (int off = 32; off > 0; off >>= 1) o += __shfl_down(o, off);
+                if (lane == 0) redr[r * 4 + wv_] = o;
+            }
+        }
+        __syncthreads();
+        if (t < 8) {
+            int n = n0 + t;
+            if (n < NDOCS) {
+                float o = redr[t * 4] + redr[t * 4 + 1] + redr[t * 4 + 2] + redr[t * 4 + 3] +
+                          outb + 0.5f * cosv[n];
+                if (isbf) ((bf16*)outv)[n] = __float2bfloat16(o);
+                else      ((float*)outv)[n] = o;
+            }
         }
     }
 }
@@ -521,8 +563,8 @@
     const void* out_b    = d_in[12];
 
     unsigned long long* maskb = (unsigned long long*)d_ws;
-    int* flag = (int*)((char*)d_ws + (size_t)4096 * 64 * 8);
-    float* f = (float*)((char*)d_ws + (size_t)4096 * 64 * 8 + 256);
+    unsigned* barr = (unsigned*)((char*)d_ws + (size_t)4096 * 64 * 8);
+    float* f = (float*)((char*)d_ws + (size_t)4096 * 64 * 8 + 2048);
     float* h       = f; f += 4096 * 256;
     float* srcb    = f; f += 4 * 4096;
     unsigned* d12g = (unsigned*)f; f += 4 * 4096;
@@ -534,25 +576,13 @@
     float* cosv    = f; f += 4096;
     float* awv     = f; f += 4096;
     float* qrow    = f; f += 256;
-    float* lpart   = f; f += 4 * 4 * 4096;
+    float* lpart   = f; f += 2 * 4 * 4096;
     ushort_t* whswz = (ushort_t*)f; f += 4096 * 256 / 2;
-    float* hnp     = f; f += (size_t)JS * 4096 * 256;
-
-    k_adjmask<<<dim3(4096), dim3(256), 0, stream>>>(adj, maskb, (const uint16_t*)emb, flag,
-                                                    dmaxu, proj_w, gat_W, fusion_w,
-                                                    projT, gatT, fwT);
-    k_proj<<<dim3(TOTAL / PR), dim3(256), 0, stream>>>(emb, proj_b, projT, h, flag);
-    k_cosupdate<<<dim3(256), dim3(256), 0, stream>>>(h);
-    for (int layer = 0; layer < 2; layer++) {
-        k_ln_wh<<<dim3(TOTAL / LR), dim3(256), 0, stream>>>(h, gatT, ln_scale, ln_bias, gat_a,
-                                                            whswz, srcb, d12g, dmaxu + layer * 1024,
-                                                            hnp, lpart, layer, layer, flag);
-        k_pv<<<dim3(TOTAL / TI, JS), dim3(512), 0, stream>>>(whswz, srcb, dmaxu + layer * 1024,
-                                                             d12g, maskb, hnp, lpart);
-    }
-    k_scores<<<dim3(256), dim3(256), 0, stream>>>(h, hnp, lpart, qrow, scoresv, cosv);
-    k_softmax<<<dim3(1), dim3(1024), 0, stream>>>(scoresv, awv);
-    k_fusion<<<dim3((NDOCS + TN - 1) / TN), dim3(256), 0, stream>>>(h, qrow, awv, cosv,
-                                                                    fwT, fusion_b, out_w,
-                                                                    out_b, (void*)d_out, flag);
-}
+    float* hnp     = f; f += (size_t)2 * 4096 * 256;
+
+    hipMemsetAsync(barr, 0, 2048, stream);
+    k_mega<<<dim3(NBLK), dim3(NTHR), 0, stream>>>(
+        adj, emb, proj_w, gat_W, fusion_w, proj_b, ln_scale, ln_bias, gat_a,
+        fusion_b, out_w, out_b, d_out, barr, maskb, dmaxu, projT, gatT, fwT,
+        h, srcb, d12g, whswz, hnp, lpart, scoresv, cosv, awv, qrow);
+}
```

Result: slower. 486.6 us (+60.1%).
